# Kernel tuning notes

Measured on AMD Instinct MI355X. Metric: run time of the kernel, lower is better.

## Reference

```python
import jax, jax.numpy as jnp
import numpy as np

SCALE = 64.0
MARGIN = 0.5
ALPHA = 1.2
SIGMA = 2.0
THRESH = float(np.cos(np.pi - MARGIN))
MM = float(np.sin(np.pi - MARGIN) * MARGIN)
IN_F, OUT_F, BATCH = 512, 100000, 512


def setup_inputs() -> dict:
    key = jax.random.key(0)
    k1, k2, k3 = jax.random.split(key, 3)
    x = jax.random.normal(k1, (BATCH, IN_F), dtype=jnp.float32)
    label = jax.random.randint(k2, (BATCH,), 0, OUT_F, dtype=jnp.int64 if jax.config.read('jax_enable_x64') else jnp.int32)
    stdv = 1.0 / np.sqrt(IN_F)
    weight = jax.random.uniform(k3, (OUT_F, IN_F), dtype=jnp.float32, minval=-stdv, maxval=stdv)
    return {"input": x, "label": label, "weight": weight}


def reference(input, label, weight):
    # row-normalize embeddings and class weights
    ex = input / jnp.linalg.norm(input, axis=1, keepdims=True)
    ew = weight / jnp.linalg.norm(weight, axis=1, keepdims=True)
    cos = jnp.einsum('bd,cd->bc', ex, ew)  # [B, C]

    b = jnp.arange(cos.shape[0])
    cos_lb = cos[b, label]  # [B] cosine at the true class
    # arcface margin: cos(theta + m) above thresh, linear fallback below
    target = jnp.where(cos_lb > THRESH,
                       jnp.cos(jnp.arccos(cos_lb) + MARGIN),
                       cos_lb - MM)  # [B]

    # negative reweighting: gaussian around the margined target (detached)
    t_scale = ALPHA * jnp.exp(-jnp.square(cos - target[:, None]) / SIGMA)
    t_scale = jax.lax.stop_gradient(t_scale)

    onehot = jax.nn.one_hot(label, cos.shape[1], dtype=cos.dtype)  # a_scale; c_scale = 1 - onehot
    logits = SCALE * (onehot * target[:, None]
                      + (1.0 - onehot) * (t_scale * cos + t_scale - 1.0))
    return logits
```

## Files before the change

### kernel.cpp

```cpp
#include <hip/hip_runtime.h>
#include <hip/hip_bf16.h>

typedef unsigned short ushort_t;
typedef unsigned int uint_t;

typedef __attribute__((ext_vector_type(8))) short short8;
typedef __attribute__((ext_vector_type(4))) float f32x4;

#define BATCH 512
#define DK    512
#define CTOT  100000
#define BN    32
#define THRESH_C (-0.8775825618903728f)
#define MM_C     (0.2397127693021015f)

static __device__ __forceinline__ ushort_t f2bf(float f) {
    union { float f; uint_t u; } v; v.f = f;
    return (ushort_t)((v.u + 0x7FFFu + ((v.u >> 16) & 1u)) >> 16);
}

__global__ __launch_bounds__(256) void arc_prep(
    const float* __restrict__ x, const int* __restrict__ label,
    const float* __restrict__ w, float* __restrict__ target,
    ushort_t* __restrict__ exbF)
{
    const int b = blockIdx.x;
    const int t = threadIdx.x;
    __shared__ float red[8];

    const float2 xv = ((const float2*)(x + (size_t)b * DK))[t];
    float ss = xv.x * xv.x + xv.y * xv.y;
    #pragma unroll
    for (int o = 32; o; o >>= 1) ss += __shfl_xor(ss, o);
    if ((t & 63) == 0) red[t >> 6] = ss;
    __syncthreads();
    const float ssx = red[0] + red[1] + red[2] + red[3];
    const float rnx = 1.0f / sqrtf(ssx);

    {
        const int k = 2 * t;
        const int ko = k >> 5;
        const int qk = (k >> 3) & 3;
        const int kj = k & 7;
        const size_t F = (size_t)(b >> 4) * 8192 + (size_t)ko * 512
                       + (size_t)qk * 128 + (size_t)(b & 15) * 8 + kj;
        ushort2 e;
        e.x = f2bf(xv.x * rnx);
        e.y = f2bf(xv.y * rnx);
        *(ushort2*)(exbF + F) = e;
    }

    const int lb = label[b];
    const float2 wv = ((const float2*)(w + (size_t)lb * DK))[t];
    float ssw = wv.x * wv.x + wv.y * wv.y;
    float dot = xv.x * wv.x + xv.y * wv.y;
    #pragma unroll
    for (int o = 32; o; o >>= 1) { ssw += __shfl_xor(ssw, o); dot += __shfl_xor(dot, o); }
    __syncthreads();
    if ((t & 63) == 0) { red[t >> 6] = ssw; red[4 + (t >> 6)] = dot; }
    __syncthreads();
    if (t == 0) {
        const float sw = red[0] + red[1] + red[2] + red[3];
        const float dt = red[4] + red[5] + red[6] + red[7];
        float cl = dt * rnx / sqrtf(sw);
        cl = fminf(fmaxf(cl, -1.0f), 1.0f);
        const float tg = (cl > THRESH_C) ? cosf(acosf(cl) + 0.5f) : (cl - MM_C);
        target[b] = tg;
    }
}

__global__ __launch_bounds__(512, 8) void arc_main(
    const ushort_t* __restrict__ exbF, const float* __restrict__ w,
    const int* __restrict__ label, const float* __restrict__ target,
    float* __restrict__ out)
{
    __shared__ ushort_t Bs[BN * DK];

    const int t    = threadIdx.x;
    const int lane = t & 63;
    const int wid  = t >> 6;
    const int c0   = blockIdx.x * BN;

    const int br  = t >> 4;
    const int bj  = t & 15;
    const float* wrow = w + (size_t)(c0 + br) * DK;
    const int s3 = br & 7;
    float bsq = 0.0f;
    #pragma unroll
    for (int i = 0; i < 8; ++i) {
        const int c = i * 64 + bj * 4;
        const float4 q = *(const float4*)(wrow + c);
        bsq += q.x * q.x + q.y * q.y + q.z * q.z + q.w * q.w;
        uint2 p;
        p.x = (uint_t)f2bf(q.x) | ((uint_t)f2bf(q.y) << 16);
        p.y = (uint_t)f2bf(q.z) | ((uint_t)f2bf(q.w) << 16);
        const int k16 = c >> 3;
        const int sw  = k16 ^ s3;
        *(uint2*)&Bs[br * DK + sw * 8 + (bj & 1) * 4] = p;
    }
    bsq += __shfl_xor(bsq, 1);
    bsq += __shfl_xor(bsq, 2);
    bsq += __shfl_xor(bsq, 4);
    bsq += __shfl_xor(bsq, 8);
    __syncthreads();

    const int m0   = wid * 64;
    const int colq = lane & 15;
    const int qk   = lane >> 4;
    const int bs3  = colq & 7;
    const ushort_t* abase = exbF + (size_t)(wid * 4) * 8192 + (size_t)lane * 8;

    f32x4 acc[4][2];
    #pragma unroll
    for (int i = 0; i < 4; ++i)
        #pragma unroll
        for (int j = 0; j < 2; ++j)
            acc[i][j] = (f32x4){0.f, 0.f, 0.f, 0.f};

    #pragma unroll 2
    for (int ko = 0; ko < 16; ++ko) {
        short8 bfr[2];
        #pragma unroll
        for (int nt = 0; nt < 2; ++nt) {
            const int idx = (nt * 16 + colq) * DK + (((ko << 2) | qk) ^ bs3) * 8;
            bfr[nt] = *(const short8*)&Bs[idx];
        }
        #pragma unroll
        for (int mt = 0; mt < 4; ++mt) {
            const short8 afr = *(const short8*)(abase + (size_t)mt * 8192 + ko * 512);
            acc[mt][0] = __builtin_amdgcn_mfma_f32_16x16x32_bf16(afr, bfr[0], acc[mt][0], 0, 0, 0);
            acc[mt][1] = __builtin_amdgcn_mfma_f32_16x16x32_bf16(afr, bfr[1], acc[mt][1], 0, 0, 0);
        }
    }

    __syncthreads();
    if (bj == 0) ((float*)Bs)[br] = 1.0f / sqrtf(bsq);
    __syncthreads();
    float rn[2];
    rn[0] = ((float*)Bs)[colq];
    rn[1] = ((float*)Bs)[16 + colq];

    #pragma unroll
    for (int mt = 0; mt < 4; ++mt) {
        #pragma unroll
        for (int rr = 0; rr < 4; ++rr) {
            const int row = m0 + mt * 16 + qk * 4 + rr;
            const float tg = target[row];
            const int   lb = label[row];
            float* orow = out + (size_t)row * CTOT + c0;
            #pragma unroll
            for (int nt = 0; nt < 2; ++nt) {
                const int cc = c0 + nt * 16 + colq;
                const float cosv = acc[mt][nt][rr] * rn[nt];
                const float d  = cosv - tg;
                const float ts = 1.2f * __expf(d * d * -0.5f);
                const float v  = (cc == lb) ? 64.0f * tg
                                            : 64.0f * (ts * cosv + ts - 1.0f);
                orow[nt * 16 + colq] = v;
            }
        }
    }
}

extern "C" void kernel_launch(void* const* d_in, const int* in_sizes, int n_in,
                              void* d_out, int out_size, void* d_ws, size_t ws_size,
                              hipStream_t stream) {
    const float* x     = (const float*)d_in[0];
    const int*   label = (const int*)d_in[1];
    const float* w     = (const float*)d_in[2];
    float* out = (float*)d_out;

    float*    target = (float*)d_ws;
    ushort_t* exbF   = (ushort_t*)((char*)d_ws + 2048);

    arc_prep<<<512, 256, 0, stream>>>(x, label, w, target, exbF);

    const int nblk = CTOT / BN;
    arc_main<<<nblk, 512, 0, stream>>>(exbF, w, label, target, out);
}
```

Measured before the change: 423.1 us.

## Pre-convert weights to bf16 fragment layout in a separate pass

Adds a kernel that normalizes and converts the weight matrix to bf16 in an MFMA-fragment-friendly layout in the workspace. The main kernel then loads B fragments directly from global memory without staging through LDS, splits each column tile across two blocks of 256 threads, and writes output with nontemporal stores. The cost is an extra full pass over the weights and a bf16 copy in the workspace, traded for halved weight bytes in the main kernel and no LDS staging or block-wide syncs. It falls back to the old LDS kernel when the workspace is too small.

```diff
diff --git a/kernel.cpp b/kernel.cpp
--- a/kernel.cpp
+++ b/kernel.cpp
@@ -69,7 +69,106 @@
     }
 }
 
-__global__ __launch_bounds__(512, 8) void arc_main(
+__global__ __launch_bounds__(256) void arc_wcvt(
+    const float* __restrict__ w, ushort_t* __restrict__ wbF,
+    float* __restrict__ rnw)
+{
+    const int rb  = blockIdx.x;
+    const int t   = threadIdx.x;
+    const int r   = t >> 4;
+    const int c16 = t & 15;
+    const int row = rb * 16 + r;
+    const float* wrow = w + (size_t)row * DK;
+    ushort_t* fbase = wbF + (size_t)rb * 8192 + (size_t)r * 8;
+
+    float ss = 0.0f;
+    #pragma unroll
+    for (int i = 0; i < 8; ++i) {
+        const int c = i * 64 + c16 * 4;
+        const float4 q = *(const float4*)(wrow + c);
+        ss += q.x * q.x + q.y * q.y + q.z * q.z + q.w * q.w;
+        ushort4 e;
+        e.x = f2bf(q.x); e.y = f2bf(q.y); e.z = f2bf(q.z); e.w = f2bf(q.w);
+        const int ko = c >> 5;
+        const int qk = (c >> 3) & 3;
+        const int j0 = c & 7;
+        *(ushort4*)(fbase + ko * 512 + qk * 128 + j0) = e;
+    }
+    ss += __shfl_xor(ss, 1);
+    ss += __shfl_xor(ss, 2);
+    ss += __shfl_xor(ss, 4);
+    ss += __shfl_xor(ss, 8);
+    if (c16 == 0) rnw[row] = 1.0f / sqrtf(ss);
+}
+
+__global__ __launch_bounds__(256, 6) void arc_main_ff(
+    const ushort_t* __restrict__ exbF, const ushort_t* __restrict__ wbF,
+    const float* __restrict__ rnw, const int* __restrict__ label,
+    const float* __restrict__ target, float* __restrict__ out)
+{
+    const int t    = threadIdx.x;
+    const int lane = t & 63;
+    const int tile = blockIdx.x >> 1;
+    const int rg   = (t >> 6) + 4 * (blockIdx.x & 1);
+    const int c0   = tile * BN;
+    const int colq = lane & 15;
+    const int qk   = lane >> 4;
+
+    const ushort_t* abase = exbF + (size_t)(rg * 4) * 8192 + (size_t)lane * 8;
+    const ushort_t* bbase = wbF + (size_t)(tile * 2) * 8192 + (size_t)lane * 8;
+
+    f32x4 acc[4][2];
+    #pragma unroll
+    for (int i = 0; i < 4; ++i)
+        #pragma unroll
+        for (int j = 0; j < 2; ++j)
+            acc[i][j] = (f32x4){0.f, 0.f, 0.f, 0.f};
+
+    #pragma unroll 4
+    for (int ko = 0; ko < 16; ++ko) {
+        const short8 b0 = *(const short8*)(bbase + ko * 512);
+        const short8 b1 = *(const short8*)(bbase + 8192 + ko * 512);
+        #pragma unroll
+        for (int mt = 0; mt < 4; ++mt) {
+            const short8 afr = *(const short8*)(abase + (size_t)mt * 8192 + ko * 512);
+            acc[mt][0] = __builtin_amdgcn_mfma_f32_16x16x32_bf16(afr, b0, acc[mt][0], 0, 0, 0);
+            acc[mt][1] = __builtin_amdgcn_mfma_f32_16x16x32_bf16(afr, b1, acc[mt][1], 0, 0, 0);
+        }
+    }
+
+    const float rn0 = rnw[c0 + colq];
+    const float rn1 = rnw[c0 + 16 + colq];
+
+    const int m0 = rg * 64;
+    #pragma unroll
+    for (int mt = 0; mt < 4; ++mt) {
+        #pragma unroll
+        for (int rr = 0; rr < 4; ++rr) {
+            const int row = m0 + mt * 16 + qk * 4 + rr;
+            const float tg = target[row];
+            const int   lb = label[row];
+            float* orow = out + (size_t)row * CTOT + c0;
+            {
+                const float cosv = acc[mt][0][rr] * rn0;
+                const float d  = cosv - tg;
+                const float ts = 1.2f * __expf(d * d * -0.5f);
+                const float v  = ((c0 + colq) == lb) ? 64.0f * tg
+                                                     : 64.0f * (ts * cosv + ts - 1.0f);
+                __builtin_nontemporal_store(v, &orow[colq]);
+            }
+            {
+                const float cosv = acc[mt][1][rr] * rn1;
+                const float d  = cosv - tg;
+                const float ts = 1.2f * __expf(d * d * -0.5f);
+                const float v  = ((c0 + 16 + colq) == lb) ? 64.0f * tg
+                                                          : 64.0f * (ts * cosv + ts - 1.0f);
+                __builtin_nontemporal_store(v, &orow[16 + colq]);
+            }
+        }
+    }
+}
+
+__global__ __launch_bounds__(512, 8) void arc_main_lds(
     const ushort_t* __restrict__ exbF, const float* __restrict__ w,
     const int* __restrict__ label, const float* __restrict__ target,
     float* __restrict__ out)
@@ -172,9 +271,16 @@
 
     float*    target = (float*)d_ws;
     ushort_t* exbF   = (ushort_t*)((char*)d_ws + 2048);
+    float*    rnw    = (float*)((char*)d_ws + 526336);
+    ushort_t* wbF    = (ushort_t*)((char*)d_ws + 935936);
+    const size_t WS_NEED = 935936 + (size_t)CTOT * DK * 2;
 
     arc_prep<<<512, 256, 0, stream>>>(x, label, w, target, exbF);
 
-    const int nblk = CTOT / BN;
-    arc_main<<<nblk, 512, 0, stream>>>(exbF, w, label, target, out);
-}
+    if (ws_size >= WS_NEED) {
+        arc_wcvt<<<CTOT / 16, 256, 0, stream>>>(w, wbF, rnw);
+        arc_main_ff<<<(CTOT / BN) * 2, 256, 0, stream>>>(exbF, wbF, rnw, label, target, out);
+    } else {
+        arc_main_lds<<<CTOT / BN, 512, 0, stream>>>(exbF, w, label, target, out);
+    }
+}
```

New measurement: 449.0 us. 6.1% more time.
